# Kernel optimization log

Hardware: AMD Instinct MI355X
Metric: run time of the kernel (lower is better)

Reference implementation:

```python
import jax, jax.numpy as jnp
import numpy as np

NEG = -9e15  # matches -9000000000000000.0 in the torch source


def setup_inputs() -> dict:
    key = jax.random.key(0)
    k1, k2, k3, k4 = jax.random.split(key, 4)
    N, F_in, F_out = 8192, 512, 64
    h = jax.random.normal(k1, (N, F_in), dtype=jnp.float32)
    adj = jax.random.randint(k2, (N, N), 0, 2, dtype=jnp.int32)
    # xavier_uniform with gain=1.414
    def xavier(k, shape, gain=1.414):
        fan_in, fan_out = shape[0], shape[1]
        bound = gain * np.sqrt(6.0 / (fan_in + fan_out))
        return jax.random.uniform(k, shape, dtype=jnp.float32, minval=-bound, maxval=bound)
    W = xavier(k3, (F_in, F_out))
    a = xavier(k4, (2 * F_out, 1))
    return {"h": h, "adj": adj, "W": W, "a": a}


def reference(h, adj, W, a):
    alpha = 0.2
    F_out = W.shape[1]
    Wh = h.astype(jnp.float32) @ W                      # [N, F_out]
    # e[i,j] = leakyrelu( Wh[i] . a[:F_out] + Wh[j] . a[F_out:] )
    Wh1 = Wh @ a[:F_out, :]                             # [N, 1]
    Wh2 = Wh @ a[F_out:, :]                             # [N, 1]
    e = jax.nn.leaky_relu(Wh1 + Wh2.T, negative_slope=alpha)  # [N, N]
    scores = jnp.where(adj > 0, e, NEG)                 # mask non-edges
    attention = jax.nn.softmax(scores, axis=1)          # row softmax
    h_prime = attention @ Wh                            # [N, F_out]
    return h_prime
```

## Files before the change

### kernel.cpp

```cpp
#include <hip/hip_runtime.h>
#include <cstdint>
#include <cstddef>


#define GAT_N    8192
#define GAT_FIN  512
#define GAT_F    64
#define TJ       64
#define JSPLIT   4
#define JCHUNK   (GAT_N / JSPLIT)
#define NTILES   (JCHUNK / TJ)

__device__ __forceinline__ float lrelu(float x) { return x > 0.f ? x : 0.2f * x; }

__global__ __launch_bounds__(256) void k_wh(
    const float* __restrict__ h, const float* __restrict__ W,
    const float* __restrict__ a,
    float* __restrict__ Wh, float* __restrict__ wh1, float* __restrict__ wh2)
{
    __shared__ float sh[16 * 516];
    const int tid = threadIdx.x;
    const size_t r0 = (size_t)blockIdx.x * 16;

    const float4* __restrict__ hsrc = (const float4*)(h + r0 * GAT_FIN);
#pragma unroll
    for (int c = 0; c < 8; ++c) {
        int idx = tid + c * 256;
        int row = idx >> 7;
        int c4  = idx & 127;
        *(float4*)&sh[row * 516 + c4 * 4] = hsrc[idx];
    }
    __syncthreads();

    const int row = tid >> 4;
    const int f4  = (tid & 15) * 4;
    float4 acc = make_float4(0.f, 0.f, 0.f, 0.f);
    const float* shr = &sh[row * 516];
#pragma unroll 8
    for (int k = 0; k < GAT_FIN; ++k) {
        float4 wv = *(const float4*)&W[k * GAT_F + f4];
        float hv = shr[k];
        acc.x += hv * wv.x; acc.y += hv * wv.y;
        acc.z += hv * wv.z; acc.w += hv * wv.w;
    }
    *(float4*)&Wh[(r0 + row) * GAT_F + f4] = acc;

    float4 a1 = *(const float4*)&a[f4];
    float4 a2 = *(const float4*)&a[GAT_F + f4];
    float pa = acc.x*a1.x + acc.y*a1.y + acc.z*a1.z + acc.w*a1.w;
    float pb = acc.x*a2.x + acc.y*a2.y + acc.z*a2.z + acc.w*a2.w;
#pragma unroll
    for (int m = 1; m < 16; m <<= 1) {
        pa += __shfl_xor(pa, m);
        pb += __shfl_xor(pb, m);
    }
    if ((tid & 15) == 0) { wh1[r0 + row] = pa; wh2[r0 + row] = pb; }
}

__global__ __launch_bounds__(256) void k_mrow(
    const float* __restrict__ wh1, const float* __restrict__ wh2,
    float* __restrict__ M)
{
    __shared__ float red[256];
    const int tid = threadIdx.x;
    float mx = -3.4e38f;
#pragma unroll
    for (int c = 0; c < GAT_N / 256; ++c) mx = fmaxf(mx, wh2[tid + c * 256]);
    red[tid] = mx;
    __syncthreads();
    for (int s = 128; s > 0; s >>= 1) {
        if (tid < s) red[tid] = fmaxf(red[tid], red[tid + s]);
        __syncthreads();
    }
    const float Mw2 = red[0];
#pragma unroll
    for (int c = 0; c < GAT_N / 256; ++c) {
        int i = tid + c * 256;
        M[i] = lrelu(wh1[i] + Mw2);
    }
}

__global__ __launch_bounds__(256) void k_attend(
    const int* __restrict__ adj, const float* __restrict__ Wh,
    const float* __restrict__ wh1, const float* __restrict__ wh2,
    const float* __restrict__ M,
    float* __restrict__ po, float* __restrict__ pl)
{
    __shared__ float sWh[2][TJ * GAT_F];
    __shared__ float sP[4][8][TJ];

    const int tid  = threadIdx.x;
    const int w    = tid >> 6;
    const int lane = tid & 63;
    const int rw   = blockIdx.x * 32 + w * 8;
    const int j0   = blockIdx.y * JCHUNK;

    const int rA   = lane >> 4;
    const int jsub = (lane & 15) * 4;
    const float a0 = wh1[rw + rA];
    const float a4 = wh1[rw + rA + 4];
    const float M0 = M[rw + rA];
    const float M4 = M[rw + rA + 4];

    const int g  = lane >> 5;
    const int fp = lane & 31;

    float2 o0 = {0.f, 0.f}, o1 = {0.f, 0.f}, o2 = {0.f, 0.f}, o3 = {0.f, 0.f};
    float l0 = 0.f, l4 = 0.f;

    {
        const float4* src = (const float4*)(Wh + (size_t)j0 * GAT_F);
#pragma unroll
        for (int c = 0; c < 4; ++c)
            ((float4*)sWh[0])[tid + c * 256] = src[tid + c * 256];
    }

    for (int t = 0; t < NTILES; ++t) {
        const int cur = t & 1;
        __syncthreads();
        if (t + 1 < NTILES) {
            const float4* src = (const float4*)(Wh + (size_t)(j0 + (t + 1) * TJ) * GAT_F);
#pragma unroll
            for (int c = 0; c < 4; ++c)
                ((float4*)sWh[cur ^ 1])[tid + c * 256] = src[tid + c * 256];
        }

        const int jt = j0 + t * TJ;
        const int4 ad0 = *(const int4*)&adj[(size_t)(rw + rA) * GAT_N + jt + jsub];
        const int4 ad4 = *(const int4*)&adj[(size_t)(rw + rA + 4) * GAT_N + jt + jsub];
        const float4 b4 = *(const float4*)&wh2[jt + jsub];
        float4 p0, p4;
        p0.x = ad0.x > 0 ? __expf(lrelu(a0 + b4.x) - M0) : 0.f;
        p0.y = ad0.y > 0 ? __expf(lrelu(a0 + b4.y) - M0) : 0.f;
        p0.z = ad0.z > 0 ? __expf(lrelu(a0 + b4.z) - M0) : 0.f;
        p0.w = ad0.w > 0 ? __expf(lrelu(a0 + b4.w) - M0) : 0.f;
        p4.x = ad4.x > 0 ? __expf(lrelu(a4 + b4.x) - M4) : 0.f;
        p4.y = ad4.y > 0 ? __expf(lrelu(a4 + b4.y) - M4) : 0.f;
        p4.z = ad4.z > 0 ? __expf(lrelu(a4 + b4.z) - M4) : 0.f;
        p4.w = ad4.w > 0 ? __expf(lrelu(a4 + b4.w) - M4) : 0.f;
        l0 += p0.x + p0.y + p0.z + p0.w;
        l4 += p4.x + p4.y + p4.z + p4.w;
        *(float4*)&sP[w][rA][jsub]     = p0;
        *(float4*)&sP[w][rA + 4][jsub] = p4;
        __builtin_amdgcn_wave_barrier();

        const float* sp0 = sP[w][g * 4 + 0];
        const float* sp1 = sP[w][g * 4 + 1];
        const float* sp2 = sP[w][g * 4 + 2];
        const float* sp3 = sP[w][g * 4 + 3];
        const float* swc = sWh[cur];
#pragma unroll
        for (int jj = 0; jj < TJ; jj += 4) {
            float4 pr0 = *(const float4*)&sp0[jj];
            float4 pr1 = *(const float4*)&sp1[jj];
            float4 pr2 = *(const float4*)&sp2[jj];
            float4 pr3 = *(const float4*)&sp3[jj];
            const float* pr0f = (const float*)&pr0;
            const float* pr1f = (const float*)&pr1;
            const float* pr2f = (const float*)&pr2;
            const float* pr3f = (const float*)&pr3;
#pragma unroll
            for (int c = 0; c < 4; ++c) {
                const float2 whv = *(const float2*)&swc[(jj + c) * GAT_F + fp * 2];
                o0.x += pr0f[c] * whv.x;  o0.y += pr0f[c] * whv.y;
                o1.x += pr1f[c] * whv.x;  o1.y += pr1f[c] * whv.y;
                o2.x += pr2f[c] * whv.x;  o2.y += pr2f[c] * whv.y;
                o3.x += pr3f[c] * whv.x;  o3.y += pr3f[c] * whv.y;
            }
        }
    }

#pragma unroll
    for (int m = 1; m < 16; m <<= 1) {
        l0 += __shfl_xor(l0, m);
        l4 += __shfl_xor(l4, m);
    }
    if ((lane & 15) == 0) {
        pl[(size_t)blockIdx.y * GAT_N + rw + rA]     = l0;
        pl[(size_t)blockIdx.y * GAT_N + rw + rA + 4] = l4;
    }
    const size_t obase = ((size_t)blockIdx.y * GAT_N + rw + g * 4) * GAT_F + fp * 2;
    *(float2*)&po[obase + 0 * GAT_F] = o0;
    *(float2*)&po[obase + 1 * GAT_F] = o1;
    *(float2*)&po[obase + 2 * GAT_F] = o2;
    *(float2*)&po[obase + 3 * GAT_F] = o3;
}

__global__ __launch_bounds__(256) void k_merge(
    const float* __restrict__ po, const float* __restrict__ pl,
    float* __restrict__ out)
{
    const int idx = blockIdx.x * 256 + threadIdx.x;
    const int i = idx >> 6;
    float s = 0.f, ls = 0.f;
#pragma unroll
    for (int y = 0; y < JSPLIT; ++y) {
        s  += po[(size_t)y * GAT_N * GAT_F + idx];
        ls += pl[(size_t)y * GAT_N + i];
    }
    out[idx] = s / ls;
}

extern "C" void kernel_launch(void* const* d_in, const int* in_sizes, int n_in,
                              void* d_out, int out_size, void* d_ws, size_t ws_size,
                              hipStream_t stream) {
    (void)in_sizes; (void)n_in; (void)out_size; (void)ws_size;
    const float* h   = (const float*)d_in[0];
    const int*   adj = (const int*)d_in[1];
    const float* W   = (const float*)d_in[2];
    const float* a   = (const float*)d_in[3];
    float* out = (float*)d_out;

    float* ws  = (float*)d_ws;
    float* Wh  = ws;
    float* wh1 = ws + 524288;
    float* wh2 = ws + 532480;
    float* M   = ws + 540672;
    float* po  = ws + 548864;
    float* pl  = ws + 2646016;

    k_wh    <<<GAT_N / 16, 256, 0, stream>>>(h, W, a, Wh, wh1, wh2);
    k_mrow  <<<1,          256, 0, stream>>>(wh1, wh2, M);
    k_attend<<<dim3(GAT_N / 32, JSPLIT), 256, 0, stream>>>(adj, Wh, wh1, wh2, M, po, pl);
    k_merge <<<GAT_N * GAT_F / 256, 256, 0, stream>>>(po, pl, out);
}
```

Measured before the change: 492.3 us.

## Fuse max-reduction into Wh kernel, re-tile attend with LDS direct loads

Removes the single-block max kernel by computing the global max of wh2 via an order-preserving integer atomicMax in k_wh, which now uses 8-row blocks with a split-K reduction. k_attend loads Wh tiles with global_load_lds into a swizzled layout, prefetches the next tile's adj and wh2 values into registers, and reorganises the P·Wh product so each lane handles 8 rows by 8 features over 8 j values, then reduces across lanes with shuffles. It also adds launch-bounds occupancy hints. In exchange, the 64 float accumulators per lane raise register pressure, the output needs cross-lane shuffle reductions, and an extra memset is added.

```diff
diff --git a/kernel.cpp b/kernel.cpp
--- a/kernel.cpp
+++ b/kernel.cpp
@@ -11,79 +11,92 @@
 #define JCHUNK   (GAT_N / JSPLIT)
 #define NTILES   (JCHUNK / TJ)
 
-__device__ __forceinline__ float lrelu(float x) { return x > 0.f ? x : 0.2f * x; }
+__device__ __forceinline__ float lrelu(float x) { return fmaxf(x, 0.2f * x); }
+
+__device__ __forceinline__ unsigned enc_f32(float f) {
+    unsigned b = __float_as_uint(f);
+    return b ^ ((b & 0x80000000u) ? 0xFFFFFFFFu : 0x80000000u);
+}
+__device__ __forceinline__ float dec_f32(unsigned u) {
+    return __uint_as_float(u ^ ((u & 0x80000000u) ? 0x80000000u : 0xFFFFFFFFu));
+}
+
+__device__ __forceinline__ void gload_lds16(const void* g, void* l) {
+    __builtin_amdgcn_global_load_lds(
+        (const __attribute__((address_space(1))) void*)g,
+        (__attribute__((address_space(3))) void*)l, 16, 0, 0);
+}
 
 __global__ __launch_bounds__(256) void k_wh(
     const float* __restrict__ h, const float* __restrict__ W,
     const float* __restrict__ a,
-    float* __restrict__ Wh, float* __restrict__ wh1, float* __restrict__ wh2)
+    float* __restrict__ Wh, float* __restrict__ wh1, float* __restrict__ wh2,
+    unsigned int* __restrict__ mw2)
 {
-    __shared__ float sh[16 * 516];
+    __shared__ float sh[8 * 516];
+    __shared__ float sacc[8 * 64];
+    __shared__ unsigned int smax[8];
     const int tid = threadIdx.x;
-    const size_t r0 = (size_t)blockIdx.x * 16;
+    const size_t r0 = (size_t)blockIdx.x * 8;
 
     const float4* __restrict__ hsrc = (const float4*)(h + r0 * GAT_FIN);
 #pragma unroll
-    for (int c = 0; c < 8; ++c) {
+    for (int c = 0; c < 4; ++c) {
         int idx = tid + c * 256;
-        int row = idx >> 7;
-        int c4  = idx & 127;
+        int row = idx >> 7, c4 = idx & 127;
         *(float4*)&sh[row * 516 + c4 * 4] = hsrc[idx];
     }
     __syncthreads();
 
-    const int row = tid >> 4;
     const int f4  = (tid & 15) * 4;
-    float4 acc = make_float4(0.f, 0.f, 0.f, 0.f);
-    const float* shr = &sh[row * 516];
-#pragma unroll 8
-    for (int k = 0; k < GAT_FIN; ++k) {
-        float4 wv = *(const float4*)&W[k * GAT_F + f4];
+    const int row = (tid >> 4) & 7;
+    const int kh  = tid >> 7;
+    float4 acc = {0.f, 0.f, 0.f, 0.f};
+    const float* shr = &sh[row * 516 + kh * 256];
+    const float* wb  = &W[(size_t)(kh * 256) * GAT_F + f4];
+#pragma unroll 4
+    for (int k = 0; k < 256; ++k) {
+        float4 wv = *(const float4*)&wb[(size_t)k * GAT_F];
         float hv = shr[k];
-        acc.x += hv * wv.x; acc.y += hv * wv.y;
-        acc.z += hv * wv.z; acc.w += hv * wv.w;
-    }
-    *(float4*)&Wh[(r0 + row) * GAT_F + f4] = acc;
-
-    float4 a1 = *(const float4*)&a[f4];
-    float4 a2 = *(const float4*)&a[GAT_F + f4];
-    float pa = acc.x*a1.x + acc.y*a1.y + acc.z*a1.z + acc.w*a1.w;
-    float pb = acc.x*a2.x + acc.y*a2.y + acc.z*a2.z + acc.w*a2.w;
-#pragma unroll
-    for (int m = 1; m < 16; m <<= 1) {
-        pa += __shfl_xor(pa, m);
-        pb += __shfl_xor(pb, m);
-    }
-    if ((tid & 15) == 0) { wh1[r0 + row] = pa; wh2[r0 + row] = pb; }
-}
-
-__global__ __launch_bounds__(256) void k_mrow(
-    const float* __restrict__ wh1, const float* __restrict__ wh2,
-    float* __restrict__ M)
-{
-    __shared__ float red[256];
-    const int tid = threadIdx.x;
-    float mx = -3.4e38f;
-#pragma unroll
-    for (int c = 0; c < GAT_N / 256; ++c) mx = fmaxf(mx, wh2[tid + c * 256]);
-    red[tid] = mx;
+        acc.x = fmaf(hv, wv.x, acc.x);
+        acc.y = fmaf(hv, wv.y, acc.y);
+        acc.z = fmaf(hv, wv.z, acc.z);
+        acc.w = fmaf(hv, wv.w, acc.w);
+    }
+    if (kh == 1) *(float4*)&sacc[(row * 16 + (tid & 15)) * 4] = acc;
     __syncthreads();
-    for (int s = 128; s > 0; s >>= 1) {
-        if (tid < s) red[tid] = fmaxf(red[tid], red[tid + s]);
-        __syncthreads();
-    }
-    const float Mw2 = red[0];
-#pragma unroll
-    for (int c = 0; c < GAT_N / 256; ++c) {
-        int i = tid + c * 256;
-        M[i] = lrelu(wh1[i] + Mw2);
-    }
-}
-
-__global__ __launch_bounds__(256) void k_attend(
+    if (kh == 0) {
+        float4 o = *(const float4*)&sacc[(row * 16 + (tid & 15)) * 4];
+        acc.x += o.x; acc.y += o.y; acc.z += o.z; acc.w += o.w;
+        *(float4*)&Wh[(r0 + row) * GAT_F + f4] = acc;
+        float4 a1 = *(const float4*)&a[f4];
+        float4 a2 = *(const float4*)&a[GAT_F + f4];
+        float pa = acc.x*a1.x + acc.y*a1.y + acc.z*a1.z + acc.w*a1.w;
+        float pb = acc.x*a2.x + acc.y*a2.y + acc.z*a2.z + acc.w*a2.w;
+#pragma unroll
+        for (int m = 1; m < 16; m <<= 1) {
+            pa += __shfl_xor(pa, m);
+            pb += __shfl_xor(pb, m);
+        }
+        if ((tid & 15) == 0) {
+            wh1[r0 + row] = pa;
+            wh2[r0 + row] = pb;
+            smax[row] = enc_f32(pb);
+        }
+    }
+    __syncthreads();
+    if (tid == 0) {
+        unsigned m = smax[0];
+#pragma unroll
+        for (int r = 1; r < 8; ++r) m = max(m, smax[r]);
+        atomicMax(mw2, m);
+    }
+}
+
+__global__ __launch_bounds__(256, 4) void k_attend(
     const int* __restrict__ adj, const float* __restrict__ Wh,
     const float* __restrict__ wh1, const float* __restrict__ wh2,
-    const float* __restrict__ M,
+    const unsigned int* __restrict__ mw2,
     float* __restrict__ po, float* __restrict__ pl)
 {
     __shared__ float sWh[2][TJ * GAT_F];
@@ -95,79 +108,101 @@
     const int rw   = blockIdx.x * 32 + w * 8;
     const int j0   = blockIdx.y * JCHUNK;
 
+    const float Mw2 = dec_f32(*mw2);
+
     const int rA   = lane >> 4;
     const int jsub = (lane & 15) * 4;
     const float a0 = wh1[rw + rA];
     const float a4 = wh1[rw + rA + 4];
-    const float M0 = M[rw + rA];
-    const float M4 = M[rw + rA + 4];
-
-    const int g  = lane >> 5;
-    const int fp = lane & 31;
-
-    float2 o0 = {0.f, 0.f}, o1 = {0.f, 0.f}, o2 = {0.f, 0.f}, o3 = {0.f, 0.f};
+    const float M0 = lrelu(a0 + Mw2);
+    const float M4 = lrelu(a4 + Mw2);
+
+    const int jb = lane >> 3, fb = lane & 7;
+    const int wrow0 = jb * 8 * GAT_F;
+    const int g0o = (((2 * fb)    ) ^ jb) * 4;
+    const int g1o = (((2 * fb) + 1) ^ jb) * 4;
+
+    int soff[4];
+#pragma unroll
+    for (int c = 0; c < 4; ++c) {
+        int G = tid + c * 256;
+        int j = G >> 4, gp = G & 15;
+        soff[c] = (j * 16 + (gp ^ (j >> 3))) * 16;
+    }
+    const int ldsoff = w * 64 * 16;
+
+    const char* wsrcb = (const char*)(Wh + (size_t)j0 * GAT_F);
+
+    const int* ap0 = adj + (size_t)(rw + rA) * GAT_N + j0 + jsub;
+    const int* ap4 = ap0 + (size_t)4 * GAT_N;
+    const float* b4p = wh2 + j0 + jsub;
+
+    {
+        char* dstb = (char*)sWh[0];
+#pragma unroll
+        for (int c = 0; c < 4; ++c)
+            gload_lds16(wsrcb + soff[c], dstb + ldsoff + c * 256 * 16);
+    }
+    int4  adjc0 = *(const int4*)ap0;
+    int4  adjc4 = *(const int4*)ap4;
+    float4 b4c  = *(const float4*)b4p;
+
+    float4 oacc[8][2] = {};
     float l0 = 0.f, l4 = 0.f;
-
-    {
-        const float4* src = (const float4*)(Wh + (size_t)j0 * GAT_F);
-#pragma unroll
-        for (int c = 0; c < 4; ++c)
-            ((float4*)sWh[0])[tid + c * 256] = src[tid + c * 256];
-    }
 
     for (int t = 0; t < NTILES; ++t) {
         const int cur = t & 1;
         __syncthreads();
+
+        const int nstep = (t + 1 < NTILES) ? (t + 1) * TJ : t * TJ;
+        int4  adjn0 = *(const int4*)(ap0 + nstep);
+        int4  adjn4 = *(const int4*)(ap4 + nstep);
+        float4 b4n  = *(const float4*)(b4p + nstep);
         if (t + 1 < NTILES) {
-            const float4* src = (const float4*)(Wh + (size_t)(j0 + (t + 1) * TJ) * GAT_F);
+            const char* src = wsrcb + (size_t)(t + 1) * (TJ * GAT_F * 4);
+            char* dstb = (char*)sWh[cur ^ 1];
 #pragma unroll
             for (int c = 0; c < 4; ++c)
-                ((float4*)sWh[cur ^ 1])[tid + c * 256] = src[tid + c * 256];
-        }
-
-        const int jt = j0 + t * TJ;
-        const int4 ad0 = *(const int4*)&adj[(size_t)(rw + rA) * GAT_N + jt + jsub];
-        const int4 ad4 = *(const int4*)&adj[(size_t)(rw + rA + 4) * GAT_N + jt + jsub];
-        const float4 b4 = *(const float4*)&wh2[jt + jsub];
+                gload_lds16(src + soff[c], dstb + ldsoff + c * 256 * 16);
+        }
+
         float4 p0, p4;
-        p0.x = ad0.x > 0 ? __expf(lrelu(a0 + b4.x) - M0) : 0.f;
-        p0.y = ad0.y > 0 ? __expf(lrelu(a0 + b4.y) - M0) : 0.f;
-        p0.z = ad0.z > 0 ? __expf(lrelu(a0 + b4.z) - M0) : 0.f;
-        p0.w = ad0.w > 0 ? __expf(lrelu(a0 + b4.w) - M0) : 0.f;
-        p4.x = ad4.x > 0 ? __expf(lrelu(a4 + b4.x) - M4) : 0.f;
-        p4.y = ad4.y > 0 ? __expf(lrelu(a4 + b4.y) - M4) : 0.f;
-        p4.z = ad4.z > 0 ? __expf(lrelu(a4 + b4.z) - M4) : 0.f;
-        p4.w = ad4.w > 0 ? __expf(lrelu(a4 + b4.w) - M4) : 0.f;
+        p0.x = adjc0.x > 0 ? __expf(lrelu(a0 + b4c.x) - M0) : 0.f;
+        p0.y = adjc0.y > 0 ? __expf(lrelu(a0 + b4c.y) - M0) : 0.f;
+        p0.z = adjc0.z > 0 ? __expf(lrelu(a0 + b4c.z) - M0) : 0.f;
+        p0.w = adjc0.w > 0 ? __expf(lrelu(a0 + b4c.w) - M0) : 0.f;
+        p4.x = adjc4.x > 0 ? __expf(lrelu(a4 + b4c.x) - M4) : 0.f;
+        p4.y = adjc4.y > 0 ? __expf(lrelu(a4 + b4c.y) - M4) : 0.f;
+        p4.z = adjc4.z > 0 ? __expf(lrelu(a4 + b4c.z) - M4) : 0.f;
+        p4.w = adjc4.w > 0 ? __expf(lrelu(a4 + b4c.w) - M4) : 0.f;
         l0 += p0.x + p0.y + p0.z + p0.w;
         l4 += p4.x + p4.y + p4.z + p4.w;
         *(float4*)&sP[w][rA][jsub]     = p0;
         *(float4*)&sP[w][rA + 4][jsub] = p4;
         __builtin_amdgcn_wave_barrier();
 
-        const float* sp0 = sP[w][g * 4 + 0];
-        const float* sp1 = sP[w][g * 4 + 1];
-        const float* sp2 = sP[w][g * 4 + 2];
-        const float* sp3 = sP[w][g * 4 + 3];
-        const float* swc = sWh[cur];
-#pragma unroll
-        for (int jj = 0; jj < TJ; jj += 4) {
-            float4 pr0 = *(const float4*)&sp0[jj];
-            float4 pr1 = *(const float4*)&sp1[jj];
-            float4 pr2 = *(const float4*)&sp2[jj];
-            float4 pr3 = *(const float4*)&sp3[jj];
-            const float* pr0f = (const float*)&pr0;
-            const float* pr1f = (const float*)&pr1;
-            const float* pr2f = (const float*)&pr2;
-            const float* pr3f = (const float*)&pr3;
-#pragma unroll
-            for (int c = 0; c < 4; ++c) {
-                const float2 whv = *(const float2*)&swc[(jj + c) * GAT_F + fp * 2];
-                o0.x += pr0f[c] * whv.x;  o0.y += pr0f[c] * whv.y;
-                o1.x += pr1f[c] * whv.x;  o1.y += pr1f[c] * whv.y;
-                o2.x += pr2f[c] * whv.x;  o2.y += pr2f[c] * whv.y;
-                o3.x += pr3f[c] * whv.x;  o3.y += pr3f[c] * whv.y;
+        const float* wb0 = &sWh[cur][wrow0 + g0o];
+        const float* wb1 = &sWh[cur][wrow0 + g1o];
+        const float* pbse = &sP[w][0][jb * 8];
+#pragma unroll
+        for (int j = 0; j < 8; ++j) {
+            float4 wv0 = *(const float4*)&wb0[j * GAT_F];
+            float4 wv1 = *(const float4*)&wb1[j * GAT_F];
+#pragma unroll
+            for (int r = 0; r < 8; ++r) {
+                float p = pbse[r * TJ + j];
+                oacc[r][0].x = fmaf(p, wv0.x, oacc[r][0].x);
+                oacc[r][0].y = fmaf(p, wv0.y, oacc[r][0].y);
+                oacc[r][0].z = fmaf(p, wv0.z, oacc[r][0].z);
+                oacc[r][0].w = fmaf(p, wv0.w, oacc[r][0].w);
+                oacc[r][1].x = fmaf(p, wv1.x, oacc[r][1].x);
+                oacc[r][1].y = fmaf(p, wv1.y, oacc[r][1].y);
+                oacc[r][1].z = fmaf(p, wv1.z, oacc[r][1].z);
+                oacc[r][1].w = fmaf(p, wv1.w, oacc[r][1].w);
             }
         }
+
+        adjc0 = adjn0; adjc4 = adjn4; b4c = b4n;
     }
 
 #pragma unroll
@@ -179,11 +214,24 @@
         pl[(size_t)blockIdx.y * GAT_N + rw + rA]     = l0;
         pl[(size_t)blockIdx.y * GAT_N + rw + rA + 4] = l4;
     }
-    const size_t obase = ((size_t)blockIdx.y * GAT_N + rw + g * 4) * GAT_F + fp * 2;
-    *(float2*)&po[obase + 0 * GAT_F] = o0;
-    *(float2*)&po[obase + 1 * GAT_F] = o1;
-    *(float2*)&po[obase + 2 * GAT_F] = o2;
-    *(float2*)&po[obase + 3 * GAT_F] = o3;
+
+    const size_t obase = ((size_t)blockIdx.y * GAT_N + rw) * GAT_F + fb * 8;
+#pragma unroll
+    for (int r = 0; r < 8; ++r) {
+#pragma unroll
+        for (int hh = 0; hh < 2; ++hh) {
+            float4 v = oacc[r][hh];
+#pragma unroll
+            for (int m = 8; m <= 32; m <<= 1) {
+                v.x += __shfl_xor(v.x, m);
+                v.y += __shfl_xor(v.y, m);
+                v.z += __shfl_xor(v.z, m);
+                v.w += __shfl_xor(v.w, m);
+            }
+            if (jb == 0)
+                *(float4*)&po[obase + (size_t)r * GAT_F + hh * 4] = v;
+        }
+    }
 }
 
 __global__ __launch_bounds__(256) void k_merge(
@@ -215,12 +263,12 @@
     float* Wh  = ws;
     float* wh1 = ws + 524288;
     float* wh2 = ws + 532480;
-    float* M   = ws + 540672;
+    unsigned int* mw2 = (unsigned int*)(ws + 540672);
     float* po  = ws + 548864;
     float* pl  = ws + 2646016;
 
-    k_wh    <<<GAT_N / 16, 256, 0, stream>>>(h, W, a, Wh, wh1, wh2);
-    k_mrow  <<<1,          256, 0, stream>>>(wh1, wh2, M);
-    k_attend<<<dim3(GAT_N / 32, JSPLIT), 256, 0, stream>>>(adj, Wh, wh1, wh2, M, po, pl);
+    hipMemsetAsync(mw2, 0, 4, stream);
+    k_wh    <<<GAT_N / 8, 256, 0, stream>>>(h, W, a, Wh, wh1, wh2, mw2);
+    k_attend<<<dim3(GAT_N / 32, JSPLIT), 256, 0, stream>>>(adj, Wh, wh1, wh2, mw2, po, pl);
     k_merge <<<GAT_N * GAT_F / 256, 256, 0, stream>>>(po, pl, out);
 }
```

After: 761.2 us. 54.6% more time.
